# Performance work log

Measured on AMD Instinct MI355X. Metric: run time of the kernel, lower is better.

Reference implementation:

```python
import jax, jax.numpy as jnp
import numpy as np


def setup_inputs() -> dict:
    key = jax.random.key(0)
    k1, k2, k3, k4, k5 = jax.random.split(key, 5)
    B, C, H, W = 8, 512, 64, 64
    mid = C // 8
    x = jax.random.normal(k1, (B, C, H, W), dtype=jnp.float32)
    # 1x1 convs (no bias) are just channel-mixing matrices
    Wb = jax.random.normal(k2, (mid, C), dtype=jnp.float32) * (1.0 / np.sqrt(C))
    Wc = jax.random.normal(k3, (mid, C), dtype=jnp.float32) * (1.0 / np.sqrt(C))
    Wd = jax.random.normal(k4, (C, C), dtype=jnp.float32) * (1.0 / np.sqrt(C))
    gamma = jax.random.normal(k5, (1,), dtype=jnp.float32)
    return {"x": x, "Wb": Wb, "Wc": Wc, "Wd": Wd, "gamma": gamma}


def reference(x, Wb, Wc, Wd, gamma):
    B, C, H, W = x.shape
    N = H * W
    xf = x.reshape(B, C, N)                          # (B, C, N)
    b = jnp.einsum('mc,bcn->bnm', Wb, xf)            # queries  (B, N, mid)
    c = jnp.einsum('mc,bcn->bmn', Wc, xf)            # keys     (B, mid, N)
    d = jnp.einsum('oc,bcn->bno', Wd, xf)            # values   (B, N, C)
    # unscaled scores, softmax over keys (last dim), as in the source
    attn = jax.nn.softmax(jnp.einsum('bnm,bmk->bnk', b, c), axis=-1)  # (B, N, N)
    out = jnp.einsum('bnk,bko->bno', attn, d)        # (B, N, C)
    out = out.transpose(0, 2, 1).reshape(B, C, H, W)
    return gamma * out + x
```

## Files before the change

### kernel.cpp

```cpp
#include <hip/hip_runtime.h>

typedef unsigned short u16;
typedef _Float16 f16x8 __attribute__((ext_vector_type(8)));
typedef short bf16x8 __attribute__((ext_vector_type(8)));
typedef float f32x16 __attribute__((ext_vector_type(16)));
typedef unsigned int u32x4 __attribute__((ext_vector_type(4)));
typedef unsigned int u32x2 __attribute__((ext_vector_type(2)));

#define LOG2E 1.44269504088896340736f

static __device__ __forceinline__ u16 f2h(float f){
  union { _Float16 h; u16 u; } v; v.h = (_Float16)f; return v.u;
}
static __device__ __forceinline__ u16 f2bf(float f){
  union { float f; unsigned u; } v; v.f = f;
  return (u16)((v.u + 0x7fffu + ((v.u >> 16) & 1u)) >> 16);
}
static __device__ __forceinline__ unsigned pk2bf(float lo, float hi){
  unsigned r; asm("v_cvt_pk_bf16_f32 %0, %1, %2" : "=v"(r) : "v"(lo), "v"(hi)); return r;
}
static __device__ __forceinline__ float ex2(float x){
#if __has_builtin(__builtin_amdgcn_exp2f)
  return __builtin_amdgcn_exp2f(x);
#else
  return exp2f(x);
#endif
}
#define PSWAP(a, b) asm("v_permlane32_swap_b32 %0, %1" : "+v"(a), "+v"(b))

typedef __attribute__((address_space(3))) unsigned int lds_u32;
typedef __attribute__((address_space(1))) const unsigned int glob_u32;
#define GLL(gp, lp) __builtin_amdgcn_global_load_lds((glob_u32*)(gp), (lds_u32*)(lp), 16, 0, 0)

__global__ __launch_bounds__(256) void k_wcvt(const float* __restrict__ wb, const float* __restrict__ wc,
                                              const float* __restrict__ wd, u16* __restrict__ w16){
  int row = blockIdx.x, t = threadIdx.x;
  const float* src; float sc;
  if (row < 512)      { src = wd + (size_t)row * 512;        sc = 1.0f;  }
  else if (row < 576) { src = wb + (size_t)(row - 512) * 512; sc = LOG2E; }
  else                { src = wc + (size_t)(row - 576) * 512; sc = 1.0f;  }
  float2 v = *(const float2*)(src + t * 2);
  unsigned pk = (unsigned)f2h(v.x * sc) | ((unsigned)f2h(v.y * sc) << 16);
  *(unsigned*)(w16 + (size_t)row * 512 + t * 2) = pk;
}

__global__ __launch_bounds__(512, 1) void k_fused(const float* __restrict__ x, const u16* __restrict__ w16,
                                                  u16* __restrict__ qkb, u16* __restrict__ vtb){
  __shared__ u16 ltmp[64 * 140];
  __shared__ u16 lx[128 * 68];
  __shared__ u16 lw[640 * 68];
  int bx = blockIdx.x;
  int b = bx >> 5, nb = bx & 31;
  int t = threadIdx.x, w = t >> 6, l = t & 63, hi = l >> 5, ln = l & 31;
  int i = w & 1, j = w >> 1;
  size_t b4096 = (size_t)b * 4096;
  f32x16 acc[5][2] = {};
  int cS = t >> 3, ncS = t & 7;
  int nT = t & 127, q4 = t >> 7;
  const float* xbase = x + ((size_t)(b * 512 + cS)) * 4096 + nb * 128 + ncS * 16;
  float4 xpre[4];
#pragma unroll
  for (int g = 0; g < 4; ++g) xpre[g] = *(const float4*)(xbase + g * 4);
  for (int kt = 0; kt < 8; ++kt) {
    int c0 = kt * 64;
    {
      u16* d = &ltmp[cS * 140 + ncS * 16];
#pragma unroll
      for (int g = 0; g < 4; ++g) {
        float4 v = xpre[g];
        unsigned lo = (unsigned)f2h(v.x) | ((unsigned)f2h(v.y) << 16);
        unsigned h2 = (unsigned)f2h(v.z) | ((unsigned)f2h(v.w) << 16);
        *(u32x2*)(d + g * 4) = u32x2{lo, h2};
      }
    }
#pragma unroll
    for (int k10 = 0; k10 < 10; ++k10) {
      int slot = t + 512 * k10;
      int row = slot >> 3, ch8 = slot & 7;
      u32x4 wv = *(const u32x4*)(w16 + (size_t)row * 512 + c0 + ch8 * 8);
      u16* d = &lw[row * 68 + ch8 * 8];
      *(u32x2*)d       = u32x2{wv[0], wv[1]};
      *(u32x2*)(d + 4) = u32x2{wv[2], wv[3]};
    }
    __syncthreads();
    if (kt < 7) {
      const float* xp = xbase + (size_t)(kt + 1) * 64 * 4096;
#pragma unroll
      for (int g = 0; g < 4; ++g) xpre[g] = *(const float4*)(xp + g * 4);
    }
    {
      u16 tmp[16];
#pragma unroll
      for (int k = 0; k < 16; ++k) tmp[k] = ltmp[(q4 * 16 + k) * 140 + nT];
      u16* d = &lx[nT * 68 + q4 * 16];
#pragma unroll
      for (int g = 0; g < 4; ++g) {
        unsigned lo = (unsigned)tmp[g * 4]     | ((unsigned)tmp[g * 4 + 1] << 16);
        unsigned h2 = (unsigned)tmp[g * 4 + 2] | ((unsigned)tmp[g * 4 + 3] << 16);
        *(u32x2*)(d + g * 4) = u32x2{lo, h2};
      }
    }
    __syncthreads();
#pragma unroll
    for (int cc = 0; cc < 4; ++cc) {
      union { u32x2 d[2]; f16x8 v; } bf[2];
#pragma unroll
      for (int u = 0; u < 2; ++u) {
        const u16* p = &lx[(i * 64 + u * 32 + ln) * 68 + cc * 16 + hi * 8];
        bf[u].d[0] = *(const u32x2*)p; bf[u].d[1] = *(const u32x2*)(p + 4);
      }
#pragma unroll
      for (int s = 0; s < 5; ++s) {
        union { u32x2 d[2]; f16x8 v; } af;
        const u16* p = &lw[(j * 160 + s * 32 + ln) * 68 + cc * 16 + hi * 8];
        af.d[0] = *(const u32x2*)p; af.d[1] = *(const u32x2*)(p + 4);
#pragma unroll
        for (int u = 0; u < 2; ++u)
          acc[s][u] = __builtin_amdgcn_mfma_f32_32x32x16_f16(af.v, bf[u].v, acc[s][u], 0, 0, 0);
      }
    }
    __syncthreads();
  }
#pragma unroll
  for (int s = 0; s < 5; ++s) {
    int rt = j * 160 + s * 32;
    if (rt < 512) {
#pragma unroll
      for (int u = 0; u < 2; ++u) {
        int n = nb * 128 + i * 64 + u * 32 + ln;
#pragma unroll
        for (int r = 0; r < 16; ++r) {
          int o = rt + (r & 3) + 8 * (r >> 2) + 4 * hi;
          vtb[((size_t)(b * 512 + o)) * 4096 + n] = f2bf(acc[s][u][r]);
        }
      }
    }
  }
  u16* qkl = lw;
  if (j == 3) {
#pragma unroll
    for (int s = 1; s < 5; ++s) {
      int mbase = (s - 1) * 32;
#pragma unroll
      for (int u = 0; u < 2; ++u) {
        int nl = i * 64 + u * 32 + ln;
#pragma unroll
        for (int r = 0; r < 16; ++r) {
          int m = mbase + (r & 3) + 8 * (r >> 2) + 4 * hi;
          qkl[nl * 132 + m] = f2h(acc[s][u][r]);
        }
      }
    }
  }
  __syncthreads();
  {
    int n2 = t >> 2, ch = t & 3;
    u16* dst = qkb + (b4096 + nb * 128 + n2) * 128 + ch * 32;
#pragma unroll
    for (int g = 0; g < 4; ++g) {
      u32x2 d0 = *(const u32x2*)(&qkl[n2 * 132 + ch * 32 + g * 8]);
      u32x2 d1 = *(const u32x2*)(&qkl[n2 * 132 + ch * 32 + g * 8 + 4]);
      *(u32x4*)(dst + g * 8) = u32x4{d0[0], d0[1], d1[0], d1[1]};
    }
  }
}

__global__ __launch_bounds__(512, 1) void k_attn2(const u16* __restrict__ qk, const u16* __restrict__ vt,
                                                  const float* __restrict__ x, const float* __restrict__ gamma,
                                                  float* __restrict__ out){
  __shared__ char smem[81920];
  int bx = blockIdx.x;
  int orig = (bx & 7) * 32 + (bx >> 3);
  int combo = orig >> 4, qt = orig & 15;
  int b = combo >> 1, oc2 = combo & 1;
  int obase = oc2 * 256;
  int t = threadIdx.x, w = t >> 6, l = t & 63, hi = l >> 5, ln = l & 31;
  int q = qt * 256 + w * 32 + ln;
  size_t b4096 = (size_t)b * 4096;
  f16x8 qf[4];
  {
    const u16* qrow = qk + (b4096 + q) * 128;
#pragma unroll
    for (int ch = 0; ch < 4; ++ch) qf[ch] = *(const f16x8*)(qrow + ch * 16 + hi * 8);
  }
  unsigned rb[4];
#pragma unroll
  for (int cc = 0; cc < 4; ++cc)
    rb[cc] = (unsigned)(ln * 128 + (((cc << 5) | (hi << 4)) ^ ((ln & 7) << 4)));
  int row = t >> 3;
  int ch2 = ((t & 7) ^ (row & 7)) * 8;
  const u16* gK = qk + (b4096 + row) * 128 + 64 + ch2;
  const u16* gV = vt + ((size_t)(b * 512 + obase + row)) * 4096 + ch2;
  unsigned ldsW = (unsigned)(w * 1024);
  GLL(gK,            smem + ldsW);
  GLL(gV,            smem + 8192  + ldsW);
  GLL(gV + 262144,   smem + 16384 + ldsW);
  GLL(gV + 524288,   smem + 24576 + ldsW);
  GLL(gV + 786432,   smem + 32768 + ldsW);
  gK += 8192; gV += 64;
  f32x16 acc[8] = {};
  float lacc = 0.0f;
  for (int kt = 0; kt < 64; ++kt) {
    __syncthreads();
    char* bufp = smem + (kt & 1) * 40960;
    if (kt < 63) {
      char* bufn = smem + ((kt + 1) & 1) * 40960;
      GLL(gK,            bufn + ldsW);
      GLL(gV,            bufn + 8192  + ldsW);
      GLL(gV + 262144,   bufn + 16384 + ldsW);
      GLL(gV + 524288,   bufn + 24576 + ldsW);
      GLL(gV + 786432,   bufn + 32768 + ldsW);
      gK += 8192; gV += 64;
    }
    f32x16 s0 = {}, s1 = {};
    __builtin_amdgcn_s_setprio(1);
#pragma unroll
    for (int cc = 0; cc < 4; ++cc) {
      f16x8 k0 = *(const f16x8*)(bufp + rb[cc]);
      f16x8 k1 = *(const f16x8*)(bufp + 4096 + rb[cc]);
      s0 = __builtin_amdgcn_mfma_f32_32x32x16_f16(k0, qf[cc], s0, 0, 0, 0);
      s1 = __builtin_amdgcn_mfma_f32_32x32x16_f16(k1, qf[cc], s1, 0, 0, 0);
    }
    __builtin_amdgcn_s_setprio(0);
#pragma unroll
    for (int r = 0; r < 16; ++r) s0[r] = ex2(s0[r]);
#pragma unroll
    for (int r = 0; r < 16; ++r) s1[r] = ex2(s1[r]);
    {
      float p[16];
#pragma unroll
      for (int r = 0; r < 16; ++r) p[r] = s0[r] + s1[r];
#pragma unroll
      for (int d = 8; d >= 1; d >>= 1)
#pragma unroll
        for (int r = 0; r < d; ++r) p[r] += p[r + d];
      lacc += p[0];
    }
    unsigned c0[8], c1[8];
#pragma unroll
    for (int ii = 0; ii < 8; ++ii) c0[ii] = pk2bf(s0[2 * ii], s0[2 * ii + 1]);
#pragma unroll
    for (int ii = 0; ii < 8; ++ii) c1[ii] = pk2bf(s1[2 * ii], s1[2 * ii + 1]);
    PSWAP(c0[0], c0[2]); PSWAP(c0[1], c0[3]); PSWAP(c0[4], c0[6]); PSWAP(c0[5], c0[7]);
    PSWAP(c1[0], c1[2]); PSWAP(c1[1], c1[3]); PSWAP(c1[4], c1[6]); PSWAP(c1[5], c1[7]);
    union U8 { unsigned u[4]; bf16x8 v; } pa[4];
#pragma unroll
    for (int jj = 0; jj < 4; ++jj) { pa[0].u[jj] = c0[jj]; pa[1].u[jj] = c0[4 + jj]; pa[2].u[jj] = c1[jj]; pa[3].u[jj] = c1[4 + jj]; }
    __builtin_amdgcn_s_setprio(1);
#pragma unroll
    for (int kc = 0; kc < 4; ++kc) {
      const char* pv = bufp + 8192 + rb[kc];
#pragma unroll
      for (int ot = 0; ot < 8; ++ot) {
        bf16x8 vb = *(const bf16x8*)(pv + ot * 4096);
        acc[ot] = __builtin_amdgcn_mfma_f32_32x32x16_bf16(pa[kc].v, vb, acc[ot], 0, 0, 0);
      }
    }
    __builtin_amdgcn_s_setprio(0);
  }
  float l_tot = lacc + __shfl_xor(lacc, 32);
  float sinv = gamma[0] / l_tot;
  __syncthreads();
  float* tb = (float*)smem + w * 1056;
#pragma unroll
  for (int ot = 0; ot < 8; ++ot) {
#pragma unroll
    for (int r = 0; r < 16; ++r) {
      int qr = (r & 3) + 8 * (r >> 2) + 4 * hi;
      tb[ln * 33 + qr] = acc[ot][r];
    }
#pragma unroll
    for (int it = 0; it < 16; ++it) {
      int orow = it * 2 + hi;
      float v = tb[orow * 33 + ln];
      size_t gi = (((size_t)(b * 512 + obase + ot * 32 + orow)) << 12) + (size_t)(qt * 256 + w * 32 + ln);
      out[gi] = sinv * v + x[gi];
    }
    __syncthreads();
  }
}

extern "C" void kernel_launch(void* const* d_in, const int* in_sizes, int n_in,
                              void* d_out, int out_size, void* d_ws, size_t ws_size,
                              hipStream_t stream) {
  (void)in_sizes; (void)n_in; (void)out_size; (void)ws_size;
  const float* x     = (const float*)d_in[0];
  const float* wb    = (const float*)d_in[1];
  const float* wc    = (const float*)d_in[2];
  const float* wd    = (const float*)d_in[3];
  const float* gamma = (const float*)d_in[4];
  float* out = (float*)d_out;
  char* ws = (char*)d_ws;
  u16* w16 = (u16*)ws;
  u16* qkb = (u16*)(ws + 1048576);
  u16* vtb = (u16*)(ws + 9437184);
  k_wcvt <<<dim3(640), dim3(256), 0, stream>>>(wb, wc, wd, w16);
  k_fused<<<dim3(256), dim3(512), 0, stream>>>(x, w16, qkb, vtb);
  k_attn2<<<dim3(256), dim3(512), 0, stream>>>(qkb, vtb, x, gamma, out);
}
```

Measured before the change: 218.3 us.

## Halve attention block threads, each wave computes two query tiles reusing K/V loads

The attention kernel now runs 256 threads (4 waves) per block instead of 512. Each wave handles 64 queries as two 32-query subtiles, so every K and V fragment read from LDS feeds two MFMAs. The exp/convert/PV step is split into per-chunk blocks so softmax work interleaves with the matrix ops. The cost is doubled accumulator registers (two sets of 8 f32x16 tiles), which raises register pressure, and fewer waves are available to hide latency.

Result: slower. 380.0 us (+74.1%).

```diff
diff --git a/kernel.cpp b/kernel.cpp
--- a/kernel.cpp
+++ b/kernel.cpp
@@ -165,7 +165,7 @@
   }
 }
 
-__global__ __launch_bounds__(512, 1) void k_attn2(const u16* __restrict__ qk, const u16* __restrict__ vt,
+__global__ __launch_bounds__(256, 1) void k_attn2(const u16* __restrict__ qk, const u16* __restrict__ vt,
                                                   const float* __restrict__ x, const float* __restrict__ gamma,
                                                   float* __restrict__ out){
   __shared__ char smem[81920];
@@ -175,13 +175,16 @@
   int b = combo >> 1, oc2 = combo & 1;
   int obase = oc2 * 256;
   int t = threadIdx.x, w = t >> 6, l = t & 63, hi = l >> 5, ln = l & 31;
-  int q = qt * 256 + w * 32 + ln;
   size_t b4096 = (size_t)b * 4096;
-  f16x8 qf[4];
+  f16x8 qf0[4], qf1[4];
   {
-    const u16* qrow = qk + (b4096 + q) * 128;
-#pragma unroll
-    for (int ch = 0; ch < 4; ++ch) qf[ch] = *(const f16x8*)(qrow + ch * 16 + hi * 8);
+    const u16* q0 = qk + (b4096 + qt * 256 + w * 64 + ln) * 128;
+    const u16* q1 = q0 + 32 * 128;
+#pragma unroll
+    for (int ch = 0; ch < 4; ++ch) {
+      qf0[ch] = *(const f16x8*)(q0 + ch * 16 + hi * 8);
+      qf1[ch] = *(const f16x8*)(q1 + ch * 16 + hi * 8);
+    }
   }
   unsigned rb[4];
 #pragma unroll
@@ -192,91 +195,103 @@
   const u16* gK = qk + (b4096 + row) * 128 + 64 + ch2;
   const u16* gV = vt + ((size_t)(b * 512 + obase + row)) * 4096 + ch2;
   unsigned ldsW = (unsigned)(w * 1024);
-  GLL(gK,            smem + ldsW);
-  GLL(gV,            smem + 8192  + ldsW);
-  GLL(gV + 262144,   smem + 16384 + ldsW);
-  GLL(gV + 524288,   smem + 24576 + ldsW);
-  GLL(gV + 786432,   smem + 32768 + ldsW);
+  {
+    char* nb_ = smem;
+    GLL(gK,           nb_ + ldsW);
+    GLL(gK + 4096,    nb_ + 4096 + ldsW);
+#pragma unroll
+    for (int i = 0; i < 8; ++i)
+      GLL(gV + i * 131072, nb_ + 8192 + i * 4096 + ldsW);
+  }
   gK += 8192; gV += 64;
-  f32x16 acc[8] = {};
-  float lacc = 0.0f;
+  f32x16 acc0[8] = {}, acc1[8] = {};
+  float lacc0 = 0.0f, lacc1 = 0.0f;
   for (int kt = 0; kt < 64; ++kt) {
     __syncthreads();
     char* bufp = smem + (kt & 1) * 40960;
     if (kt < 63) {
-      char* bufn = smem + ((kt + 1) & 1) * 40960;
-      GLL(gK,            bufn + ldsW);
-      GLL(gV,            bufn + 8192  + ldsW);
-      GLL(gV + 262144,   bufn + 16384 + ldsW);
-      GLL(gV + 524288,   bufn + 24576 + ldsW);
-      GLL(gV + 786432,   bufn + 32768 + ldsW);
+      char* nb_ = smem + ((kt + 1) & 1) * 40960;
+      GLL(gK,           nb_ + ldsW);
+      GLL(gK + 4096,    nb_ + 4096 + ldsW);
+#pragma unroll
+      for (int i = 0; i < 8; ++i)
+        GLL(gV + i * 131072, nb_ + 8192 + i * 4096 + ldsW);
       gK += 8192; gV += 64;
     }
-    f32x16 s0 = {}, s1 = {};
+    f32x16 s00 = {}, s01 = {}, s10 = {}, s11 = {};
     __builtin_amdgcn_s_setprio(1);
 #pragma unroll
     for (int cc = 0; cc < 4; ++cc) {
       f16x8 k0 = *(const f16x8*)(bufp + rb[cc]);
       f16x8 k1 = *(const f16x8*)(bufp + 4096 + rb[cc]);
-      s0 = __builtin_amdgcn_mfma_f32_32x32x16_f16(k0, qf[cc], s0, 0, 0, 0);
-      s1 = __builtin_amdgcn_mfma_f32_32x32x16_f16(k1, qf[cc], s1, 0, 0, 0);
+      s00 = __builtin_amdgcn_mfma_f32_32x32x16_f16(k0, qf0[cc], s00, 0, 0, 0);
+      s10 = __builtin_amdgcn_mfma_f32_32x32x16_f16(k0, qf1[cc], s10, 0, 0, 0);
+      s01 = __builtin_amdgcn_mfma_f32_32x32x16_f16(k1, qf0[cc], s01, 0, 0, 0);
+      s11 = __builtin_amdgcn_mfma_f32_32x32x16_f16(k1, qf1[cc], s11, 0, 0, 0);
     }
     __builtin_amdgcn_s_setprio(0);
-#pragma unroll
-    for (int r = 0; r < 16; ++r) s0[r] = ex2(s0[r]);
-#pragma unroll
-    for (int r = 0; r < 16; ++r) s1[r] = ex2(s1[r]);
-    {
-      float p[16];
-#pragma unroll
-      for (int r = 0; r < 16; ++r) p[r] = s0[r] + s1[r];
-#pragma unroll
-      for (int d = 8; d >= 1; d >>= 1)
-#pragma unroll
-        for (int r = 0; r < d; ++r) p[r] += p[r + d];
-      lacc += p[0];
-    }
-    unsigned c0[8], c1[8];
-#pragma unroll
-    for (int ii = 0; ii < 8; ++ii) c0[ii] = pk2bf(s0[2 * ii], s0[2 * ii + 1]);
-#pragma unroll
-    for (int ii = 0; ii < 8; ++ii) c1[ii] = pk2bf(s1[2 * ii], s1[2 * ii + 1]);
-    PSWAP(c0[0], c0[2]); PSWAP(c0[1], c0[3]); PSWAP(c0[4], c0[6]); PSWAP(c0[5], c0[7]);
-    PSWAP(c1[0], c1[2]); PSWAP(c1[1], c1[3]); PSWAP(c1[4], c1[6]); PSWAP(c1[5], c1[7]);
-    union U8 { unsigned u[4]; bf16x8 v; } pa[4];
-#pragma unroll
-    for (int jj = 0; jj < 4; ++jj) { pa[0].u[jj] = c0[jj]; pa[1].u[jj] = c0[4 + jj]; pa[2].u[jj] = c1[jj]; pa[3].u[jj] = c1[4 + jj]; }
-    __builtin_amdgcn_s_setprio(1);
-#pragma unroll
-    for (int kc = 0; kc < 4; ++kc) {
-      const char* pv = bufp + 8192 + rb[kc];
+    float psum0 = 0.0f, psum1 = 0.0f;
+#pragma unroll
+    for (int blk = 0; blk < 4; ++blk) {
+      const int base = (blk & 1) * 8;
+      f32x16& sva = (blk < 2) ? s00 : s01;
+      f32x16& svb = (blk < 2) ? s10 : s11;
+      float e0[8], e1[8];
+#pragma unroll
+      for (int jj = 0; jj < 8; ++jj) e0[jj] = ex2(sva[base + jj]);
+#pragma unroll
+      for (int jj = 0; jj < 8; ++jj) e1[jj] = ex2(svb[base + jj]);
+      psum0 += ((e0[0] + e0[1]) + (e0[2] + e0[3])) + ((e0[4] + e0[5]) + (e0[6] + e0[7]));
+      psum1 += ((e1[0] + e1[1]) + (e1[2] + e1[3])) + ((e1[4] + e1[5]) + (e1[6] + e1[7]));
+      unsigned ca[4], cb[4];
+      ca[0] = pk2bf(e0[0], e0[1]); ca[1] = pk2bf(e0[2], e0[3]);
+      ca[2] = pk2bf(e0[4], e0[5]); ca[3] = pk2bf(e0[6], e0[7]);
+      cb[0] = pk2bf(e1[0], e1[1]); cb[1] = pk2bf(e1[2], e1[3]);
+      cb[2] = pk2bf(e1[4], e1[5]); cb[3] = pk2bf(e1[6], e1[7]);
+      PSWAP(ca[0], ca[2]); PSWAP(ca[1], ca[3]);
+      PSWAP(cb[0], cb[2]); PSWAP(cb[1], cb[3]);
+      union U8 { unsigned u[4]; bf16x8 v; } pa0, pa1;
+      pa0.u[0] = ca[0]; pa0.u[1] = ca[1]; pa0.u[2] = ca[2]; pa0.u[3] = ca[3];
+      pa1.u[0] = cb[0]; pa1.u[1] = cb[1]; pa1.u[2] = cb[2]; pa1.u[3] = cb[3];
+      const char* pv = bufp + 8192 + rb[blk];
+      __builtin_amdgcn_s_setprio(1);
 #pragma unroll
       for (int ot = 0; ot < 8; ++ot) {
         bf16x8 vb = *(const bf16x8*)(pv + ot * 4096);
-        acc[ot] = __builtin_amdgcn_mfma_f32_32x32x16_bf16(pa[kc].v, vb, acc[ot], 0, 0, 0);
-      }
-    }
-    __builtin_amdgcn_s_setprio(0);
-  }
-  float l_tot = lacc + __shfl_xor(lacc, 32);
-  float sinv = gamma[0] / l_tot;
+        acc0[ot] = __builtin_amdgcn_mfma_f32_32x32x16_bf16(pa0.v, vb, acc0[ot], 0, 0, 0);
+        acc1[ot] = __builtin_amdgcn_mfma_f32_32x32x16_bf16(pa1.v, vb, acc1[ot], 0, 0, 0);
+      }
+      __builtin_amdgcn_s_setprio(0);
+    }
+    lacc0 += psum0; lacc1 += psum1;
+  }
+  float g = gamma[0];
+  float l0 = lacc0 + __shfl_xor(lacc0, 32);
+  float l1 = lacc1 + __shfl_xor(lacc1, 32);
+  float sinv0 = g / l0, sinv1 = g / l1;
   __syncthreads();
   float* tb = (float*)smem + w * 1056;
 #pragma unroll
-  for (int ot = 0; ot < 8; ++ot) {
-#pragma unroll
-    for (int r = 0; r < 16; ++r) {
-      int qr = (r & 3) + 8 * (r >> 2) + 4 * hi;
-      tb[ln * 33 + qr] = acc[ot][r];
-    }
-#pragma unroll
-    for (int it = 0; it < 16; ++it) {
-      int orow = it * 2 + hi;
-      float v = tb[orow * 33 + ln];
-      size_t gi = (((size_t)(b * 512 + obase + ot * 32 + orow)) << 12) + (size_t)(qt * 256 + w * 32 + ln);
-      out[gi] = sinv * v + x[gi];
-    }
-    __syncthreads();
+  for (int qs = 0; qs < 2; ++qs) {
+    float sv = qs ? sinv1 : sinv0;
+    size_t qcol = (size_t)(qt * 256 + w * 64 + qs * 32 + ln);
+#pragma unroll
+    for (int ot = 0; ot < 8; ++ot) {
+      f32x16& av = qs ? acc1[ot] : acc0[ot];
+#pragma unroll
+      for (int r = 0; r < 16; ++r) {
+        int qr = (r & 3) + 8 * (r >> 2) + 4 * hi;
+        tb[ln * 33 + qr] = av[r];
+      }
+#pragma unroll
+      for (int it = 0; it < 16; ++it) {
+        int orow = it * 2 + hi;
+        float v = tb[orow * 33 + ln];
+        size_t gi = (((size_t)(b * 512 + obase + ot * 32 + orow)) << 12) + qcol;
+        out[gi] = sv * v + x[gi];
+      }
+      __syncthreads();
+    }
   }
 }
 
@@ -296,5 +311,5 @@
   u16* vtb = (u16*)(ws + 9437184);
   k_wcvt <<<dim3(640), dim3(256), 0, stream>>>(wb, wc, wd, w16);
   k_fused<<<dim3(256), dim3(512), 0, stream>>>(x, w16, qkb, vtb);
-  k_attn2<<<dim3(256), dim3(512), 0, stream>>>(qkb, vtb, x, gamma, out);
-}
+  k_attn2<<<dim3(256), dim3(256), 0, stream>>>(qkb, vtb, x, gamma, out);
+}
```
